# Kernel tuning notes

Hardware: AMD Instinct MI355X
Metric: run time of the kernel (lower is better)

Reference implementation:

```python
import jax, jax.numpy as jnp
import numpy as np

N_VERTICES = 1_000_000
N_EDGES = 16_000_000


def setup_inputs() -> dict:
    key = jax.random.key(0)
    k1, k2, k3 = jax.random.split(key, 3)
    vertex_attr = jax.random.normal(k1, (N_VERTICES, 2), dtype=jnp.float32)
    edgeij_pair = jax.random.randint(k2, (2, N_EDGES), 0, N_VERTICES, dtype=jnp.int64)
    edge_attr = jax.random.normal(k3, (N_EDGES, 2), dtype=jnp.float32)
    g = jnp.zeros((1, 1), dtype=jnp.float32)
    batch = jnp.zeros((N_VERTICES,), dtype=jnp.int64)
    return {"vertex_attr": vertex_attr, "edgeij_pair": edgeij_pair,
            "edge_attr": edge_attr, "g": g, "batch": batch}


def reference(vertex_attr, edgeij_pair, edge_attr, g, batch):
    # c_ij: second edge feature column, [E, 1]
    c_ij = edge_attr[:, 1:2]
    b_i = vertex_attr[:, 0:1]  # [N, 1]
    x_i = vertex_attr[:, 1:2]  # [N, 1]
    n_vertices = x_i.shape[0]
    # edge-to-vertex aggregation: sum c_ij into receiving vertex i (row 0)
    cbar_i = jax.ops.segment_sum(c_ij, edgeij_pair[0], num_segments=n_vertices)
    r_i = b_i - cbar_i
    return jnp.concatenate([b_i, x_i, r_i], axis=1)  # [N, 3]
```

## Files before the change

### kernel.cpp

```cpp
#include <hip/hip_runtime.h>


#define BSHIFT 11
#define BSIZE (1 << BSHIFT)
#define NBUCK_PAD 512
#define TILE 8192
#define TPB 512

__global__ __launch_bounds__(TPB, 2)
void vu_partition(const int* __restrict__ src,
                  const float* __restrict__ eattr,
                  unsigned long long* __restrict__ pairs,
                  unsigned int* __restrict__ alloc,
                  int ne, int nbuck, int cap) {
    __shared__ unsigned long long sorted[TILE];
    __shared__ unsigned int hist[NBUCK_PAD];
    __shared__ unsigned int base_l[NBUCK_PAD];
    __shared__ unsigned int cursor[NBUCK_PAD];
    __shared__ unsigned int gbase[NBUCK_PAD];

    int t = threadIdx.x;
    int tile0 = blockIdx.x * TILE;
    int lim = ne - tile0; if (lim > TILE) lim = TILE;

    hist[t] = 0u;
    __syncthreads();

    for (int i = t; i < lim; i += TPB)
        atomicAdd(&hist[src[tile0 + i] >> BSHIFT], 1u);
    __syncthreads();

    unsigned int mycnt = hist[t];
    for (int off = 1; off < NBUCK_PAD; off <<= 1) {
        unsigned int v = (t >= off) ? hist[t - off] : 0u;
        __syncthreads();
        hist[t] += v;
        __syncthreads();
    }
    unsigned int excl = hist[t] - mycnt;
    base_l[t] = excl;
    cursor[t] = excl;
    gbase[t] = (t < nbuck && mycnt) ? atomicAdd(&alloc[t], mycnt) : 0u;
    __syncthreads();

    for (int i = t; i < lim; i += TPB) {
        int e = tile0 + i;
        int s = src[e];
        float2 ec = ((const float2*)eattr)[e];
        unsigned int pos = atomicAdd(&cursor[s >> BSHIFT], 1u);
        sorted[pos] =
            ((unsigned long long)__float_as_uint(ec.y) << 32) | (unsigned int)s;
    }
    __syncthreads();

    for (int i = t; i < lim; i += TPB) {
        unsigned long long p = sorted[i];
        unsigned int q = ((unsigned int)p) >> BSHIFT;
        unsigned int dst = q * (unsigned int)cap + gbase[q]
                         + ((unsigned int)i - base_l[q]);
        unsigned int hi = q * (unsigned int)cap + (unsigned int)cap - 1u;
        if (dst > hi) dst = hi;
        pairs[dst] = p;
    }
}

__global__ __launch_bounds__(1024, 2)
void vu_aggregate(const unsigned long long* __restrict__ pairs,
                  const unsigned int* __restrict__ alloc,
                  const float* __restrict__ vattr,
                  float* __restrict__ out,
                  int nv, int cap) {
    __shared__ float acc[BSIZE];
    int q = blockIdx.x;
    int t = threadIdx.x;
    for (int i = t; i < BSIZE; i += 1024) acc[i] = 0.0f;
    __syncthreads();

    unsigned int cnt = alloc[q];
    if (cnt > (unsigned int)cap) cnt = (unsigned int)cap;
    const unsigned long long* p = pairs + (size_t)q * (size_t)cap;
    for (unsigned int i = t; i < cnt; i += 1024) {
        unsigned long long v = p[i];
        atomicAdd(&acc[((unsigned int)v) & (BSIZE - 1)],
                  __uint_as_float((unsigned int)(v >> 32)));
    }
    __syncthreads();

    int v0 = q << BSHIFT;
    for (int i = t; i < BSIZE; i += 1024) {
        int v = v0 + i;
        if (v < nv) {
            float2 va = ((const float2*)vattr)[v];
            out[3 * v + 0] = va.x;
            out[3 * v + 1] = va.y;
            out[3 * v + 2] = va.x - acc[i];
        }
    }
}

__global__ void vu_init_kernel(const float* __restrict__ vattr,
                               float* __restrict__ out, int n) {
    int i = blockIdx.x * blockDim.x + threadIdx.x;
    if (i < n) {
        float2 v = ((const float2*)vattr)[i];
        out[3 * i + 0] = v.x;
        out[3 * i + 1] = v.y;
        out[3 * i + 2] = v.x;
    }
}

__global__ void vu_scatter_kernel(const int* __restrict__ src,
                                  const float* __restrict__ eattr,
                                  float* __restrict__ out, int ne) {
    int t = blockIdx.x * blockDim.x + threadIdx.x;
    int e0 = t * 4;
    if (e0 + 3 < ne) {
        int4 idx = ((const int4*)src)[t];
        float4 a = ((const float4*)eattr)[2 * t + 0];
        float4 b = ((const float4*)eattr)[2 * t + 1];
        atomicAdd(&out[3 * idx.x + 2], -a.y);
        atomicAdd(&out[3 * idx.y + 2], -a.w);
        atomicAdd(&out[3 * idx.z + 2], -b.y);
        atomicAdd(&out[3 * idx.w + 2], -b.w);
    } else {
        for (int e = e0; e < ne; ++e)
            atomicAdd(&out[3 * src[e] + 2], -eattr[2 * e + 1]);
    }
}

extern "C" void kernel_launch(void* const* d_in, const int* in_sizes, int n_in,
                              void* d_out, int out_size, void* d_ws, size_t ws_size,
                              hipStream_t stream) {
    const float* vattr = (const float*)d_in[0];
    const int* edges = (const int*)d_in[1];
    const float* eattr = (const float*)d_in[2];
    float* out = (float*)d_out;

    int nv = in_sizes[0] / 2;
    int ne = in_sizes[2] / 2;

    int nbuck = (nv + BSIZE - 1) >> BSHIFT;
    int mean = ne / nbuck;
    int cap = mean + mean / 8 + 1024;
    cap = (cap + 15) & ~15;

    size_t alloc_bytes = 4096;
    size_t pair_bytes = (size_t)nbuck * (size_t)cap * 8ull;
    size_t need = alloc_bytes + pair_bytes;

    if (ws_size >= need && nbuck <= NBUCK_PAD) {
        unsigned int* alloc = (unsigned int*)d_ws;
        unsigned long long* pairs = (unsigned long long*)((char*)d_ws + alloc_bytes);
        (void)hipMemsetAsync(alloc, 0, (size_t)nbuck * 4, stream);

        int p1_blocks = (ne + TILE - 1) / TILE;
        vu_partition<<<p1_blocks, TPB, 0, stream>>>(edges, eattr, pairs, alloc,
                                                    ne, nbuck, cap);
        vu_aggregate<<<nbuck, 1024, 0, stream>>>(pairs, alloc, vattr, out, nv, cap);
    } else {
        int threads = 256;
        int blocks = (nv + threads - 1) / threads;
        vu_init_kernel<<<blocks, threads, 0, stream>>>(vattr, out, nv);
        int nt = (ne + 3) / 4;
        blocks = (nt + threads - 1) / threads;
        vu_scatter_kernel<<<blocks, threads, 0, stream>>>(edges, eattr, out, ne);
    }
}
```

Measured before the change: 429.3 us.

## Vectorize partition loads, widen blocks, and stage aggregate output through LDS

The partition kernel moves to 1024 threads per block, and full tiles load source indices and edge attributes with int4/float4 vector loads that are kept in registers and reused between the histogram pass and the scatter pass. The aggregate kernel reads pairs two at a time as 128-bit loads. It then writes its output rows into a shared-memory buffer and stores that buffer to global memory as coalesced float4 writes, replacing the strided 3-float stores. The extra 24KB of LDS in aggregate and the larger partition blocks may reduce occupancy.

```diff
diff --git a/kernel.cpp b/kernel.cpp
--- a/kernel.cpp
+++ b/kernel.cpp
@@ -5,9 +5,9 @@
 #define BSIZE (1 << BSHIFT)
 #define NBUCK_PAD 512
 #define TILE 8192
-#define TPB 512
-
-__global__ __launch_bounds__(TPB, 2)
+#define TPB 1024
+
+__global__ __launch_bounds__(TPB, 8)
 void vu_partition(const int* __restrict__ src,
                   const float* __restrict__ eattr,
                   unsigned long long* __restrict__ pairs,
@@ -22,35 +22,71 @@
     int t = threadIdx.x;
     int tile0 = blockIdx.x * TILE;
     int lim = ne - tile0; if (lim > TILE) lim = TILE;
-
-    hist[t] = 0u;
-    __syncthreads();
-
-    for (int i = t; i < lim; i += TPB)
-        atomicAdd(&hist[src[tile0 + i] >> BSHIFT], 1u);
-    __syncthreads();
-
-    unsigned int mycnt = hist[t];
+    bool full = (lim == TILE);
+
+    if (t < NBUCK_PAD) hist[t] = 0u;
+    __syncthreads();
+
+    int4 sA, sB;
+    if (full) {
+        const int4* s4 = (const int4*)(src + tile0);
+        sA = s4[t];
+        sB = s4[t + TPB];
+        atomicAdd(&hist[((unsigned)sA.x) >> BSHIFT], 1u);
+        atomicAdd(&hist[((unsigned)sA.y) >> BSHIFT], 1u);
+        atomicAdd(&hist[((unsigned)sA.z) >> BSHIFT], 1u);
+        atomicAdd(&hist[((unsigned)sA.w) >> BSHIFT], 1u);
+        atomicAdd(&hist[((unsigned)sB.x) >> BSHIFT], 1u);
+        atomicAdd(&hist[((unsigned)sB.y) >> BSHIFT], 1u);
+        atomicAdd(&hist[((unsigned)sB.z) >> BSHIFT], 1u);
+        atomicAdd(&hist[((unsigned)sB.w) >> BSHIFT], 1u);
+    } else {
+        for (int i = t; i < lim; i += TPB)
+            atomicAdd(&hist[((unsigned)src[tile0 + i]) >> BSHIFT], 1u);
+    }
+    __syncthreads();
+
+    unsigned int mycnt = (t < NBUCK_PAD) ? hist[t] : 0u;
     for (int off = 1; off < NBUCK_PAD; off <<= 1) {
-        unsigned int v = (t >= off) ? hist[t - off] : 0u;
+        unsigned int v = 0u;
+        if (t < NBUCK_PAD && t >= off) v = hist[t - off];
         __syncthreads();
-        hist[t] += v;
+        if (t < NBUCK_PAD) hist[t] += v;
         __syncthreads();
     }
-    unsigned int excl = hist[t] - mycnt;
-    base_l[t] = excl;
-    cursor[t] = excl;
-    gbase[t] = (t < nbuck && mycnt) ? atomicAdd(&alloc[t], mycnt) : 0u;
-    __syncthreads();
-
-    for (int i = t; i < lim; i += TPB) {
-        int e = tile0 + i;
-        int s = src[e];
-        float2 ec = ((const float2*)eattr)[e];
-        unsigned int pos = atomicAdd(&cursor[s >> BSHIFT], 1u);
-        sorted[pos] =
-            ((unsigned long long)__float_as_uint(ec.y) << 32) | (unsigned int)s;
-    }
+    if (t < NBUCK_PAD) {
+        unsigned int excl = hist[t] - mycnt;
+        base_l[t] = excl;
+        cursor[t] = excl;
+        gbase[t] = (t < nbuck && mycnt) ? atomicAdd(&alloc[t], mycnt) : 0u;
+    }
+    __syncthreads();
+
+#define VU_SCAT(sv, cv) do { \
+        unsigned int q_ = ((unsigned)(sv)) >> BSHIFT; \
+        unsigned int pos_ = atomicAdd(&cursor[q_], 1u); \
+        sorted[pos_] = ((unsigned long long)__float_as_uint(cv) << 32) \
+                       | (unsigned)(sv); } while (0)
+    if (full) {
+        const float4* ef = (const float4*)eattr;
+        int b0 = (tile0 >> 1) + 2 * t;
+        float4 cA0 = ef[b0];
+        float4 cA1 = ef[b0 + 1];
+        float4 cB0 = ef[b0 + 2048];
+        float4 cB1 = ef[b0 + 2049];
+        VU_SCAT(sA.x, cA0.y); VU_SCAT(sA.y, cA0.w);
+        VU_SCAT(sA.z, cA1.y); VU_SCAT(sA.w, cA1.w);
+        VU_SCAT(sB.x, cB0.y); VU_SCAT(sB.y, cB0.w);
+        VU_SCAT(sB.z, cB1.y); VU_SCAT(sB.w, cB1.w);
+    } else {
+        for (int i = t; i < lim; i += TPB) {
+            int e = tile0 + i;
+            int s = src[e];
+            float2 ec = ((const float2*)eattr)[e];
+            VU_SCAT(s, ec.y);
+        }
+    }
+#undef VU_SCAT
     __syncthreads();
 
     for (int i = t; i < lim; i += TPB) {
@@ -64,37 +100,62 @@
     }
 }
 
-__global__ __launch_bounds__(1024, 2)
+__global__ __launch_bounds__(1024)
 void vu_aggregate(const unsigned long long* __restrict__ pairs,
                   const unsigned int* __restrict__ alloc,
                   const float* __restrict__ vattr,
                   float* __restrict__ out,
                   int nv, int cap) {
     __shared__ float acc[BSIZE];
+    __shared__ float obuf[BSIZE * 3];
     int q = blockIdx.x;
     int t = threadIdx.x;
-    for (int i = t; i < BSIZE; i += 1024) acc[i] = 0.0f;
+    acc[t] = 0.0f;
+    acc[t + 1024] = 0.0f;
     __syncthreads();
 
     unsigned int cnt = alloc[q];
     if (cnt > (unsigned int)cap) cnt = (unsigned int)cap;
     const unsigned long long* p = pairs + (size_t)q * (size_t)cap;
-    for (unsigned int i = t; i < cnt; i += 1024) {
-        unsigned long long v = p[i];
+    const ulonglong2* p2 = (const ulonglong2*)p;
+    unsigned int n2 = cnt >> 1;
+    for (unsigned int i = t; i < n2; i += 1024) {
+        ulonglong2 v = p2[i];
+        atomicAdd(&acc[((unsigned int)v.x) & (BSIZE - 1)],
+                  __uint_as_float((unsigned int)(v.x >> 32)));
+        atomicAdd(&acc[((unsigned int)v.y) & (BSIZE - 1)],
+                  __uint_as_float((unsigned int)(v.y >> 32)));
+    }
+    if (t == 0 && (cnt & 1u)) {
+        unsigned long long v = p[cnt - 1];
         atomicAdd(&acc[((unsigned int)v) & (BSIZE - 1)],
                   __uint_as_float((unsigned int)(v >> 32)));
     }
     __syncthreads();
 
     int v0 = q << BSHIFT;
-    for (int i = t; i < BSIZE; i += 1024) {
+#pragma unroll
+    for (int k = 0; k < 2; ++k) {
+        int i = t + k * 1024;
         int v = v0 + i;
         if (v < nv) {
             float2 va = ((const float2*)vattr)[v];
-            out[3 * v + 0] = va.x;
-            out[3 * v + 1] = va.y;
-            out[3 * v + 2] = va.x - acc[i];
+            obuf[3 * i + 0] = va.x;
+            obuf[3 * i + 1] = va.y;
+            obuf[3 * i + 2] = va.x - acc[i];
         }
+    }
+    __syncthreads();
+
+    long fbase = (long)q * (BSIZE * 3);
+    int nfl = 3 * nv - (int)fbase;
+    if (nfl > BSIZE * 3) nfl = BSIZE * 3;
+    if (nfl > 0) {
+        float4* o4 = (float4*)(out + fbase);
+        const float4* s4 = (const float4*)obuf;
+        int n4 = nfl >> 2;
+        for (int j = t; j < n4; j += 1024) o4[j] = s4[j];
+        for (int j = (n4 << 2) + t; j < nfl; j += 1024) out[fbase + j] = obuf[j];
     }
 }
 
```

Result: faster. 400.0 us (-6.8%).
